# Performance work log

Measured on AMD Instinct MI355X. Metric: run time of the kernel, lower is better.

The kernel has to match this reference:

```python
import jax, jax.numpy as jnp
import numpy as np

ALPHA = 0.2  # LeakyReLU negative slope
NEG_PAD = jnp.float32(-2**31)
N, IN_F, OUT_F = 8192, 512, 64


def setup_inputs() -> dict:
    key = jax.random.key(0)
    k1, k2, k3, k4 = jax.random.split(key, 4)
    h = jax.random.normal(k1, (N, IN_F), dtype=jnp.float32)
    adj = jax.random.randint(k2, (N, N), 0, 2, dtype=jnp.int32)
    # xavier_uniform with gain=1.414
    gain = 1.414
    limW = gain * np.sqrt(6.0 / (IN_F + OUT_F))
    W = jax.random.uniform(k3, (IN_F, OUT_F), dtype=jnp.float32, minval=-limW, maxval=limW)
    lima = gain * np.sqrt(6.0 / (2 * OUT_F + 1))
    a = jax.random.uniform(k4, (2 * OUT_F, 1), dtype=jnp.float32, minval=-lima, maxval=lima)
    return {"h": h, "adj": adj, "W": W, "a": a}


def reference(h, adj, W, a):
    Wh = h @ W                                   # [N, F']
    Wh1 = Wh @ a[:OUT_F, :]                      # [N, 1]
    Wh2 = Wh @ a[OUT_F:, :]                      # [N, 1]
    e = jax.nn.leaky_relu(Wh1 + Wh2.T, negative_slope=ALPHA)  # [N, N]
    attention = jnp.where(adj > 0, e, NEG_PAD)
    attention = jax.nn.softmax(attention, axis=1)
    # dropout in eval mode -> identity
    h_prime = attention @ Wh                     # [N, F']
    return jax.nn.elu(h_prime)                   # concat=True branch
```

## Files before the change

### kernel.cpp

```cpp
#include <hip/hip_runtime.h>
#include <cstdint>
#include <cstddef>

#define LRALPHA 0.2f

typedef _Float16 half8 __attribute__((ext_vector_type(8)));
typedef float f32x4 __attribute__((ext_vector_type(4)));

__global__ __launch_bounds__(256) void k1_wh(
    const float* __restrict__ h, const float* __restrict__ W, const float* __restrict__ a,
    _Float16* __restrict__ whT, float* __restrict__ wh1, float* __restrict__ wh2)
{
  __shared__ __align__(16) float h_lds[32][34];
  __shared__ __align__(16) float w_lds[32][64];
  __shared__ __align__(16) _Float16 whT_l[64][32];

  const int t = threadIdx.x;
  const int tx = t & 15, ty = t >> 4;
  const int i0 = blockIdx.x * 32;

  const int hrow = t >> 3, hk4 = (t & 7) * 4;
  const int wk = t >> 3, wc = (t & 7) * 8;

  float acc00 = 0, acc01 = 0, acc02 = 0, acc03 = 0;
  float acc10 = 0, acc11 = 0, acc12 = 0, acc13 = 0;

  float4 hv  = *reinterpret_cast<const float4*>(&h[(size_t)(i0 + hrow) * 512 + hk4]);
  float4 wv0 = *reinterpret_cast<const float4*>(&W[(size_t)wk * 64 + wc]);
  float4 wv1 = *reinterpret_cast<const float4*>(&W[(size_t)wk * 64 + wc + 4]);

  for (int k0 = 0; k0 < 512; k0 += 32) {
    h_lds[hk4 + 0][hrow] = hv.x;
    h_lds[hk4 + 1][hrow] = hv.y;
    h_lds[hk4 + 2][hrow] = hv.z;
    h_lds[hk4 + 3][hrow] = hv.w;
    *reinterpret_cast<float4*>(&w_lds[wk][wc])     = wv0;
    *reinterpret_cast<float4*>(&w_lds[wk][wc + 4]) = wv1;
    __syncthreads();
    if (k0 + 32 < 512) {
      hv  = *reinterpret_cast<const float4*>(&h[(size_t)(i0 + hrow) * 512 + k0 + 32 + hk4]);
      wv0 = *reinterpret_cast<const float4*>(&W[(size_t)(k0 + 32 + wk) * 64 + wc]);
      wv1 = *reinterpret_cast<const float4*>(&W[(size_t)(k0 + 32 + wk) * 64 + wc + 4]);
    }
#pragma unroll
    for (int kk = 0; kk < 32; ++kk) {
      float2 av = *reinterpret_cast<const float2*>(&h_lds[kk][ty * 2]);
      float4 bv = *reinterpret_cast<const float4*>(&w_lds[kk][tx * 4]);
      acc00 += av.x * bv.x; acc01 += av.x * bv.y; acc02 += av.x * bv.z; acc03 += av.x * bv.w;
      acc10 += av.y * bv.x; acc11 += av.y * bv.y; acc12 += av.y * bv.z; acc13 += av.y * bv.w;
    }
    __syncthreads();
  }

  const float a10 = a[tx * 4 + 0], a11 = a[tx * 4 + 1], a12 = a[tx * 4 + 2], a13 = a[tx * 4 + 3];
  const float a20 = a[64 + tx * 4 + 0], a21 = a[64 + tx * 4 + 1], a22 = a[64 + tx * 4 + 2], a23 = a[64 + tx * 4 + 3];
  float s1_0 = acc00 * a10 + acc01 * a11 + acc02 * a12 + acc03 * a13;
  float s1_1 = acc10 * a10 + acc11 * a11 + acc12 * a12 + acc13 * a13;
  float s2_0 = acc00 * a20 + acc01 * a21 + acc02 * a22 + acc03 * a23;
  float s2_1 = acc10 * a20 + acc11 * a21 + acc12 * a22 + acc13 * a23;
#pragma unroll
  for (int m = 1; m < 16; m <<= 1) {
    s1_0 += __shfl_xor(s1_0, m); s1_1 += __shfl_xor(s1_1, m);
    s2_0 += __shfl_xor(s2_0, m); s2_1 += __shfl_xor(s2_1, m);
  }
  if (tx == 0) {
    wh1[i0 + ty * 2 + 0] = s1_0; wh1[i0 + ty * 2 + 1] = s1_1;
    wh2[i0 + ty * 2 + 0] = s2_0; wh2[i0 + ty * 2 + 1] = s2_1;
  }

  whT_l[tx * 4 + 0][ty * 2 + 0] = (_Float16)acc00;
  whT_l[tx * 4 + 1][ty * 2 + 0] = (_Float16)acc01;
  whT_l[tx * 4 + 2][ty * 2 + 0] = (_Float16)acc02;
  whT_l[tx * 4 + 3][ty * 2 + 0] = (_Float16)acc03;
  whT_l[tx * 4 + 0][ty * 2 + 1] = (_Float16)acc10;
  whT_l[tx * 4 + 1][ty * 2 + 1] = (_Float16)acc11;
  whT_l[tx * 4 + 2][ty * 2 + 1] = (_Float16)acc12;
  whT_l[tx * 4 + 3][ty * 2 + 1] = (_Float16)acc13;
  __syncthreads();
  {
    const int c = t >> 2, r8 = (t & 3) * 8;
    half8 v = *reinterpret_cast<const half8*>(&whT_l[c][r8]);
    *reinterpret_cast<half8*>(&whT[(size_t)c * 8192 + i0 + r8]) = v;
  }
}

__global__ __launch_bounds__(256) void k1b_max(const float* __restrict__ wh2,
                                               float* __restrict__ G)
{
  const int t = threadIdx.x;
  float m = -1e30f;
  for (int i = t; i < 8192; i += 256) m = fmaxf(m, wh2[i]);
#pragma unroll
  for (int mask = 32; mask >= 1; mask >>= 1) m = fmaxf(m, __shfl_xor(m, mask));
  __shared__ float wm[4];
  if ((t & 63) == 0) wm[t >> 6] = m;
  __syncthreads();
  if (t == 0) G[0] = fmaxf(fmaxf(wm[0], wm[1]), fmaxf(wm[2], wm[3]));
}

__global__ __launch_bounds__(256) void k2_attn(
    const int* __restrict__ adj, const _Float16* __restrict__ whT,
    const float* __restrict__ wh1, const float* __restrict__ wh2,
    const float* __restrict__ Gp, float* __restrict__ out)
{
  __shared__ __align__(16) float Osm[4][16][64];
  __shared__ float Dsm[4][16];

  const int t = threadIdx.x;
  const int lane = t & 63;
  const int w = t >> 6;
  const int c = lane & 15;
  const int ks = lane >> 4;
  const int i0 = blockIdx.x * 16;

  const float Gv = Gp[0];
  const float w1r = wh1[i0 + c];
  const float mx = w1r + Gv;
  const float mh = fmaxf(mx, LRALPHA * mx);

  const int*      adjp = adj + (size_t)(i0 + c) * 8192 + w * 2048 + ks * 8;
  const float*    wh2p = wh2 + w * 2048 + ks * 8;
  const _Float16* bp0  = whT + (size_t)c * 8192 + w * 2048 + ks * 8;
  const _Float16* bp1  = bp0 + (size_t)16 * 8192;
  const _Float16* bp2  = bp0 + (size_t)32 * 8192;
  const _Float16* bp3  = bp0 + (size_t)48 * 8192;

  f32x4 acc0 = {0.f,0.f,0.f,0.f}, acc1 = {0.f,0.f,0.f,0.f};
  f32x4 acc2 = {0.f,0.f,0.f,0.f}, acc3 = {0.f,0.f,0.f,0.f};
  float ps = 0.f;

  int4 Aa0, Aa1, Ba0, Ba1;
  float4 Aw0, Aw1, Bw0, Bw1;
  half8 Ab0, Ab1, Ab2, Ab3, Bb0, Bb1, Bb2, Bb3;

#define LOADSET(P, CI) do { const int jj_ = (CI) * 32;                          \
    P##a0 = *reinterpret_cast<const int4*>(adjp + jj_);                         \
    P##a1 = *reinterpret_cast<const int4*>(adjp + jj_ + 4);                     \
    P##w0 = *reinterpret_cast<const float4*>(wh2p + jj_);                       \
    P##w1 = *reinterpret_cast<const float4*>(wh2p + jj_ + 4);                   \
    P##b0 = *reinterpret_cast<const half8*>(bp0 + jj_);                         \
    P##b1 = *reinterpret_cast<const half8*>(bp1 + jj_);                         \
    P##b2 = *reinterpret_cast<const half8*>(bp2 + jj_);                         \
    P##b3 = *reinterpret_cast<const half8*>(bp3 + jj_); } while (0)

#define BODY(P, NEXTCI) do {                                                    \
    const int4 ca0 = P##a0, ca1 = P##a1;                                        \
    const float4 cw0 = P##w0, cw1 = P##w1;                                      \
    const half8 cb0 = P##b0, cb1 = P##b1, cb2 = P##b2, cb3 = P##b3;             \
    if ((NEXTCI) < 64) LOADSET(P, NEXTCI);                                      \
    half8 af;                                                                   \
    { float s_ = w1r + cw0.x; s_ = fmaxf(s_, LRALPHA*s_);                       \
      float p_ = (ca0.x > 0) ? __expf(s_ - mh) : 0.f; ps += p_; af[0] = (_Float16)p_; } \
    { float s_ = w1r + cw0.y; s_ = fmaxf(s_, LRALPHA*s_);                       \
      float p_ = (ca0.y > 0) ? __expf(s_ - mh) : 0.f; ps += p_; af[1] = (_Float16)p_; } \
    { float s_ = w1r + cw0.z; s_ = fmaxf(s_, LRALPHA*s_);                       \
      float p_ = (ca0.z > 0) ? __expf(s_ - mh) : 0.f; ps += p_; af[2] = (_Float16)p_; } \
    { float s_ = w1r + cw0.w; s_ = fmaxf(s_, LRALPHA*s_);                       \
      float p_ = (ca0.w > 0) ? __expf(s_ - mh) : 0.f; ps += p_; af[3] = (_Float16)p_; } \
    { float s_ = w1r + cw1.x; s_ = fmaxf(s_, LRALPHA*s_);                       \
      float p_ = (ca1.x > 0) ? __expf(s_ - mh) : 0.f; ps += p_; af[4] = (_Float16)p_; } \
    { float s_ = w1r + cw1.y; s_ = fmaxf(s_, LRALPHA*s_);                       \
      float p_ = (ca1.y > 0) ? __expf(s_ - mh) : 0.f; ps += p_; af[5] = (_Float16)p_; } \
    { float s_ = w1r + cw1.z; s_ = fmaxf(s_, LRALPHA*s_);                       \
      float p_ = (ca1.z > 0) ? __expf(s_ - mh) : 0.f; ps += p_; af[6] = (_Float16)p_; } \
    { float s_ = w1r + cw1.w; s_ = fmaxf(s_, LRALPHA*s_);                       \
      float p_ = (ca1.w > 0) ? __expf(s_ - mh) : 0.f; ps += p_; af[7] = (_Float16)p_; } \
    acc0 = __builtin_amdgcn_mfma_f32_16x16x32_f16(af, cb0, acc0, 0, 0, 0);      \
    acc1 = __builtin_amdgcn_mfma_f32_16x16x32_f16(af, cb1, acc1, 0, 0, 0);      \
    acc2 = __builtin_amdgcn_mfma_f32_16x16x32_f16(af, cb2, acc2, 0, 0, 0);      \
    acc3 = __builtin_amdgcn_mfma_f32_16x16x32_f16(af, cb3, acc3, 0, 0, 0);      \
  } while (0)

  LOADSET(A, 0);
  LOADSET(B, 1);

  for (int ci = 0; ci < 64; ci += 2) {
    BODY(A, ci + 2);
    BODY(B, ci + 3);
  }
#undef BODY
#undef LOADSET

  float r = ps;
  r += __shfl_xor(r, 16);
  r += __shfl_xor(r, 32);
  if (ks == 0) Dsm[w][c] = r;

#pragma unroll
  for (int q = 0; q < 4; ++q) {
    Osm[w][ks * 4 + q][ 0 + c] = acc0[q];
    Osm[w][ks * 4 + q][16 + c] = acc1[q];
    Osm[w][ks * 4 + q][32 + c] = acc2[q];
    Osm[w][ks * 4 + q][48 + c] = acc3[q];
  }
  __syncthreads();

  {
    const int row = t >> 4, c4 = (t & 15) * 4;
    float4 v0 = *reinterpret_cast<const float4*>(&Osm[0][row][c4]);
    float4 v1 = *reinterpret_cast<const float4*>(&Osm[1][row][c4]);
    float4 v2 = *reinterpret_cast<const float4*>(&Osm[2][row][c4]);
    float4 v3 = *reinterpret_cast<const float4*>(&Osm[3][row][c4]);
    const float d = Dsm[0][row] + Dsm[1][row] + Dsm[2][row] + Dsm[3][row];
    const float inv = 1.0f / d;
    float4 o;
    o.x = (v0.x + v1.x + v2.x + v3.x) * inv;
    o.y = (v0.y + v1.y + v2.y + v3.y) * inv;
    o.z = (v0.z + v1.z + v2.z + v3.z) * inv;
    o.w = (v0.w + v1.w + v2.w + v3.w) * inv;
    o.x = o.x > 0.f ? o.x : __expf(o.x) - 1.f;
    o.y = o.y > 0.f ? o.y : __expf(o.y) - 1.f;
    o.z = o.z > 0.f ? o.z : __expf(o.z) - 1.f;
    o.w = o.w > 0.f ? o.w : __expf(o.w) - 1.f;
    *reinterpret_cast<float4*>(&out[(size_t)(i0 + row) * 64 + c4]) = o;
  }
}

extern "C" void kernel_launch(void* const* d_in, const int* in_sizes, int n_in,
                              void* d_out, int out_size, void* d_ws, size_t ws_size,
                              hipStream_t stream) {
  const float* h   = (const float*)d_in[0];
  const int*   adj = (const int*)d_in[1];
  const float* W   = (const float*)d_in[2];
  const float* a   = (const float*)d_in[3];
  float* out = (float*)d_out;

  char* ws = (char*)d_ws;
  _Float16* whT = (_Float16*)ws;
  float* wh1 = (float*)(ws + (1 << 20));
  float* wh2 = (float*)(ws + (1 << 20) + 32768);
  float* G   = (float*)(ws + (1 << 20) + 65536);

  k1_wh<<<dim3(256), dim3(256), 0, stream>>>(h, W, a, whT, wh1, wh2);
  k1b_max<<<dim3(1), dim3(256), 0, stream>>>(wh2, G);
  k2_attn<<<dim3(512), dim3(256), 0, stream>>>(adj, whT, wh1, wh2, G, out);
}
```

Before: 133.5 us.

## Split attention neighbour range across blocks and combine partials in separate kernel

Each k2_attn block now runs 8 waves over 128 rows and a single quarter of the neighbour (j) range, so all waves in a block share the same whT and wh2 slice. Previously each block's 4 waves covered 16 rows across all four j quarters. Unnormalized output and denominator partials go to global workspace, and a new k3_combine kernel sums the four partials and applies the normalization and ELU. The aim is better cache reuse of the B operand and wh2. The cost is an extra kernel launch and roughly 8 MB of partial writes plus reads.

```diff
diff --git a/kernel.cpp b/kernel.cpp
--- a/kernel.cpp
+++ b/kernel.cpp
@@ -98,29 +98,28 @@
   if (t == 0) G[0] = fmaxf(fmaxf(wm[0], wm[1]), fmaxf(wm[2], wm[3]));
 }
 
-__global__ __launch_bounds__(256) void k2_attn(
+__global__ __launch_bounds__(512) void k2_attn(
     const int* __restrict__ adj, const _Float16* __restrict__ whT,
     const float* __restrict__ wh1, const float* __restrict__ wh2,
-    const float* __restrict__ Gp, float* __restrict__ out)
-{
-  __shared__ __align__(16) float Osm[4][16][64];
-  __shared__ float Dsm[4][16];
-
+    const float* __restrict__ Gp, float* __restrict__ Opart, float* __restrict__ Dpart)
+{
   const int t = threadIdx.x;
   const int lane = t & 63;
   const int w = t >> 6;
   const int c = lane & 15;
   const int ks = lane >> 4;
-  const int i0 = blockIdx.x * 16;
+  const int bj = blockIdx.x & 3;
+  const int bi = blockIdx.x >> 2;
+  const int row0 = bi * 128 + w * 16;
 
   const float Gv = Gp[0];
-  const float w1r = wh1[i0 + c];
+  const float w1r = wh1[row0 + c];
   const float mx = w1r + Gv;
   const float mh = fmaxf(mx, LRALPHA * mx);
 
-  const int*      adjp = adj + (size_t)(i0 + c) * 8192 + w * 2048 + ks * 8;
-  const float*    wh2p = wh2 + w * 2048 + ks * 8;
-  const _Float16* bp0  = whT + (size_t)c * 8192 + w * 2048 + ks * 8;
+  const int*      adjp = adj + (size_t)(row0 + c) * 8192 + bj * 2048 + ks * 8;
+  const float*    wh2p = wh2 + bj * 2048 + ks * 8;
+  const _Float16* bp0  = whT + (size_t)c * 8192 + bj * 2048 + ks * 8;
   const _Float16* bp1  = bp0 + (size_t)16 * 8192;
   const _Float16* bp2  = bp0 + (size_t)32 * 8192;
   const _Float16* bp3  = bp0 + (size_t)48 * 8192;
@@ -184,36 +183,44 @@
   float r = ps;
   r += __shfl_xor(r, 16);
   r += __shfl_xor(r, 32);
-  if (ks == 0) Dsm[w][c] = r;
-
+  if (ks == 0) Dpart[(size_t)bj * 8192 + row0 + c] = r;
+
+  float* ob = Opart + ((size_t)bj * 8192 + row0 + ks * 4) * 64;
 #pragma unroll
   for (int q = 0; q < 4; ++q) {
-    Osm[w][ks * 4 + q][ 0 + c] = acc0[q];
-    Osm[w][ks * 4 + q][16 + c] = acc1[q];
-    Osm[w][ks * 4 + q][32 + c] = acc2[q];
-    Osm[w][ks * 4 + q][48 + c] = acc3[q];
-  }
-  __syncthreads();
-
-  {
-    const int row = t >> 4, c4 = (t & 15) * 4;
-    float4 v0 = *reinterpret_cast<const float4*>(&Osm[0][row][c4]);
-    float4 v1 = *reinterpret_cast<const float4*>(&Osm[1][row][c4]);
-    float4 v2 = *reinterpret_cast<const float4*>(&Osm[2][row][c4]);
-    float4 v3 = *reinterpret_cast<const float4*>(&Osm[3][row][c4]);
-    const float d = Dsm[0][row] + Dsm[1][row] + Dsm[2][row] + Dsm[3][row];
-    const float inv = 1.0f / d;
-    float4 o;
-    o.x = (v0.x + v1.x + v2.x + v3.x) * inv;
-    o.y = (v0.y + v1.y + v2.y + v3.y) * inv;
-    o.z = (v0.z + v1.z + v2.z + v3.z) * inv;
-    o.w = (v0.w + v1.w + v2.w + v3.w) * inv;
-    o.x = o.x > 0.f ? o.x : __expf(o.x) - 1.f;
-    o.y = o.y > 0.f ? o.y : __expf(o.y) - 1.f;
-    o.z = o.z > 0.f ? o.z : __expf(o.z) - 1.f;
-    o.w = o.w > 0.f ? o.w : __expf(o.w) - 1.f;
-    *reinterpret_cast<float4*>(&out[(size_t)(i0 + row) * 64 + c4]) = o;
-  }
+    ob[(size_t)q * 64 +  0 + c] = acc0[q];
+    ob[(size_t)q * 64 + 16 + c] = acc1[q];
+    ob[(size_t)q * 64 + 32 + c] = acc2[q];
+    ob[(size_t)q * 64 + 48 + c] = acc3[q];
+  }
+}
+
+__global__ __launch_bounds__(256) void k3_combine(
+    const float* __restrict__ Opart, const float* __restrict__ Dpart,
+    float* __restrict__ out)
+{
+  const int idx = blockIdx.x * 256 + threadIdx.x;
+  const int row = idx >> 4, c4 = (idx & 15) * 4;
+
+  const float d = Dpart[row] + Dpart[8192 + row] + Dpart[2 * 8192 + row] + Dpart[3 * 8192 + row];
+  const float inv = 1.0f / d;
+
+  const size_t o = (size_t)row * 64 + c4;
+  float4 v0 = *reinterpret_cast<const float4*>(&Opart[o]);
+  float4 v1 = *reinterpret_cast<const float4*>(&Opart[(size_t)8192 * 64 + o]);
+  float4 v2 = *reinterpret_cast<const float4*>(&Opart[(size_t)2 * 8192 * 64 + o]);
+  float4 v3 = *reinterpret_cast<const float4*>(&Opart[(size_t)3 * 8192 * 64 + o]);
+
+  float4 r;
+  r.x = (v0.x + v1.x + v2.x + v3.x) * inv;
+  r.y = (v0.y + v1.y + v2.y + v3.y) * inv;
+  r.z = (v0.z + v1.z + v2.z + v3.z) * inv;
+  r.w = (v0.w + v1.w + v2.w + v3.w) * inv;
+  r.x = r.x > 0.f ? r.x : __expf(r.x) - 1.f;
+  r.y = r.y > 0.f ? r.y : __expf(r.y) - 1.f;
+  r.z = r.z > 0.f ? r.z : __expf(r.z) - 1.f;
+  r.w = r.w > 0.f ? r.w : __expf(r.w) - 1.f;
+  *reinterpret_cast<float4*>(&out[o]) = r;
 }
 
 extern "C" void kernel_launch(void* const* d_in, const int* in_sizes, int n_in,
@@ -227,11 +234,14 @@
 
   char* ws = (char*)d_ws;
   _Float16* whT = (_Float16*)ws;
-  float* wh1 = (float*)(ws + (1 << 20));
-  float* wh2 = (float*)(ws + (1 << 20) + 32768);
-  float* G   = (float*)(ws + (1 << 20) + 65536);
+  float* wh1  = (float*)(ws + 0x100000);
+  float* wh2  = (float*)(ws + 0x108000);
+  float* G    = (float*)(ws + 0x110000);
+  float* Dpart = (float*)(ws + 0x110100);
+  float* Opart = (float*)(ws + 0x140000);
 
   k1_wh<<<dim3(256), dim3(256), 0, stream>>>(h, W, a, whT, wh1, wh2);
   k1b_max<<<dim3(1), dim3(256), 0, stream>>>(wh2, G);
-  k2_attn<<<dim3(512), dim3(256), 0, stream>>>(adj, whT, wh1, wh2, G, out);
-}
+  k2_attn<<<dim3(256), dim3(512), 0, stream>>>(adj, whT, wh1, wh2, G, Opart, Dpart);
+  k3_combine<<<dim3(512), dim3(256), 0, stream>>>(Opart, Dpart, out);
+}
```

Result: no change. 132.8 us (-0.5%).

## Bit-pack adjacency in a pre-pass and read compact mask in attention kernel

Applied to the files above, without the earlier changes.

Adds a pre-pass that compresses the int32 adjacency matrix into one bit per entry, so the attention kernel reads an 8 MB mask instead of the full int matrix. The fp16 Wh transpose is stored in a swizzled chunk layout so each wave's B-operand loads are contiguous. The attention kernel moves to 512 threads with 8 waves splitting the key dimension. The full adjacency is still read once by the pack kernel, and an extra launch plus mask write is added.

```diff
diff --git a/kernel.cpp b/kernel.cpp
--- a/kernel.cpp
+++ b/kernel.cpp
@@ -7,9 +7,25 @@
 typedef _Float16 half8 __attribute__((ext_vector_type(8)));
 typedef float f32x4 __attribute__((ext_vector_type(4)));
 
+__global__ __launch_bounds__(256) void k0_bitpack(const int* __restrict__ adj,
+                                                  unsigned char* __restrict__ bits8)
+{
+  const int nb = 8192 * 1024;
+  const int stride = gridDim.x * 256;
+  for (int b = blockIdx.x * 256 + threadIdx.x; b < nb; b += stride) {
+    const int4* p = reinterpret_cast<const int4*>(adj + (size_t)b * 8);
+    const int4 x = p[0], y = p[1];
+    unsigned m = (x.x > 0 ? 1u : 0u) | (x.y > 0 ? 2u : 0u)
+               | (x.z > 0 ? 4u : 0u) | (x.w > 0 ? 8u : 0u)
+               | (y.x > 0 ? 16u : 0u) | (y.y > 0 ? 32u : 0u)
+               | (y.z > 0 ? 64u : 0u) | (y.w > 0 ? 128u : 0u);
+    bits8[b] = (unsigned char)m;
+  }
+}
+
 __global__ __launch_bounds__(256) void k1_wh(
     const float* __restrict__ h, const float* __restrict__ W, const float* __restrict__ a,
-    _Float16* __restrict__ whT, float* __restrict__ wh1, float* __restrict__ wh2)
+    _Float16* __restrict__ whTsw, float* __restrict__ wh1, float* __restrict__ wh2)
 {
   __shared__ __align__(16) float h_lds[32][34];
   __shared__ __align__(16) float w_lds[32][64];
@@ -78,9 +94,9 @@
   whT_l[tx * 4 + 3][ty * 2 + 1] = (_Float16)acc13;
   __syncthreads();
   {
-    const int c = t >> 2, r8 = (t & 3) * 8;
-    half8 v = *reinterpret_cast<const half8*>(&whT_l[c][r8]);
-    *reinterpret_cast<half8*>(&whT[(size_t)c * 8192 + i0 + r8]) = v;
+    const int cp = t >> 6, cc = (t >> 2) & 15, ks = t & 3;
+    half8 v = *reinterpret_cast<const half8*>(&whT_l[cp * 16 + cc][ks * 8]);
+    *reinterpret_cast<half8*>(&whTsw[(size_t)(i0 >> 5) * 2048 + cp * 512 + (cc * 4 + ks) * 8]) = v;
   }
 }
 
@@ -98,13 +114,13 @@
   if (t == 0) G[0] = fmaxf(fmaxf(wm[0], wm[1]), fmaxf(wm[2], wm[3]));
 }
 
-__global__ __launch_bounds__(256) void k2_attn(
-    const int* __restrict__ adj, const _Float16* __restrict__ whT,
+__global__ __launch_bounds__(512) void k2_attn(
+    const unsigned char* __restrict__ bits8, const _Float16* __restrict__ whTsw,
     const float* __restrict__ wh1, const float* __restrict__ wh2,
     const float* __restrict__ Gp, float* __restrict__ out)
 {
-  __shared__ __align__(16) float Osm[4][16][64];
-  __shared__ float Dsm[4][16];
+  __shared__ __align__(16) float Osm[8][16][64];
+  __shared__ float Dsm[8][16];
 
   const int t = threadIdx.x;
   const int lane = t & 63;
@@ -118,53 +134,49 @@
   const float mx = w1r + Gv;
   const float mh = fmaxf(mx, LRALPHA * mx);
 
-  const int*      adjp = adj + (size_t)(i0 + c) * 8192 + w * 2048 + ks * 8;
-  const float*    wh2p = wh2 + w * 2048 + ks * 8;
-  const _Float16* bp0  = whT + (size_t)c * 8192 + w * 2048 + ks * 8;
-  const _Float16* bp1  = bp0 + (size_t)16 * 8192;
-  const _Float16* bp2  = bp0 + (size_t)32 * 8192;
-  const _Float16* bp3  = bp0 + (size_t)48 * 8192;
+  const unsigned char* mp = bits8 + (size_t)(i0 + c) * 1024 + w * 128 + ks;
+  const float* wh2p = wh2 + w * 1024 + ks * 8;
+  const _Float16* bp = whTsw + (size_t)(w * 32) * 2048 + (c * 4 + ks) * 8;
 
   f32x4 acc0 = {0.f,0.f,0.f,0.f}, acc1 = {0.f,0.f,0.f,0.f};
   f32x4 acc2 = {0.f,0.f,0.f,0.f}, acc3 = {0.f,0.f,0.f,0.f};
   float ps = 0.f;
 
-  int4 Aa0, Aa1, Ba0, Ba1;
+  unsigned Am, Bm;
   float4 Aw0, Aw1, Bw0, Bw1;
   half8 Ab0, Ab1, Ab2, Ab3, Bb0, Bb1, Bb2, Bb3;
 
-#define LOADSET(P, CI) do { const int jj_ = (CI) * 32;                          \
-    P##a0 = *reinterpret_cast<const int4*>(adjp + jj_);                         \
-    P##a1 = *reinterpret_cast<const int4*>(adjp + jj_ + 4);                     \
-    P##w0 = *reinterpret_cast<const float4*>(wh2p + jj_);                       \
-    P##w1 = *reinterpret_cast<const float4*>(wh2p + jj_ + 4);                   \
-    P##b0 = *reinterpret_cast<const half8*>(bp0 + jj_);                         \
-    P##b1 = *reinterpret_cast<const half8*>(bp1 + jj_);                         \
-    P##b2 = *reinterpret_cast<const half8*>(bp2 + jj_);                         \
-    P##b3 = *reinterpret_cast<const half8*>(bp3 + jj_); } while (0)
+#define LOADSET(P, CI) do {                                                     \
+    P##m  = mp[(CI) * 4];                                                       \
+    P##w0 = *reinterpret_cast<const float4*>(wh2p + (CI) * 32);                 \
+    P##w1 = *reinterpret_cast<const float4*>(wh2p + (CI) * 32 + 4);             \
+    P##b0 = *reinterpret_cast<const half8*>(bp + (size_t)(CI) * 2048);          \
+    P##b1 = *reinterpret_cast<const half8*>(bp + (size_t)(CI) * 2048 + 512);    \
+    P##b2 = *reinterpret_cast<const half8*>(bp + (size_t)(CI) * 2048 + 1024);   \
+    P##b3 = *reinterpret_cast<const half8*>(bp + (size_t)(CI) * 2048 + 1536); } while (0)
 
 #define BODY(P, NEXTCI) do {                                                    \
-    const int4 ca0 = P##a0, ca1 = P##a1;                                        \
+    const unsigned cm = P##m;                                                   \
     const float4 cw0 = P##w0, cw1 = P##w1;                                      \
     const half8 cb0 = P##b0, cb1 = P##b1, cb2 = P##b2, cb3 = P##b3;             \
-    if ((NEXTCI) < 64) LOADSET(P, NEXTCI);                                      \
+    if ((NEXTCI) < 32) LOADSET(P, NEXTCI);                                      \
     half8 af;                                                                   \
     { float s_ = w1r + cw0.x; s_ = fmaxf(s_, LRALPHA*s_);                       \
-      float p_ = (ca0.x > 0) ? __expf(s_ - mh) : 0.f; ps += p_; af[0] = (_Float16)p_; } \
+      float p_ = (cm & 1u)   ? __expf(s_ - mh) : 0.f; ps += p_; af[0] = (_Float16)p_; } \
     { float s_ = w1r + cw0.y; s_ = fmaxf(s_, LRALPHA*s_);                       \
-      float p_ = (ca0.y > 0) ? __expf(s_ - mh) : 0.f; ps += p_; af[1] = (_Float16)p_; } \
+      float p_ = (cm & 2u)   ? __expf(s_ - mh) : 0.f; ps += p_; af[1] = (_Float16)p_; } \
     { float s_ = w1r + cw0.z; s_ = fmaxf(s_, LRALPHA*s_);                       \
-      float p_ = (ca0.z > 0) ? __expf(s_ - mh) : 0.f; ps += p_; af[2] = (_Float16)p_; } \
+      float p_ = (cm & 4u)   ? __expf(s_ - mh) : 0.f; ps += p_; af[2] = (_Float16)p_; } \
     { float s_ = w1r + cw0.w; s_ = fmaxf(s_, LRALPHA*s_);                       \
-      float p_ = (ca0.w > 0) ? __expf(s_ - mh) : 0.f; ps += p_; af[3] = (_Float16)p_; } \
+      float p_ = (cm & 8u)   ? __expf(s_ - mh) : 0.f; ps += p_; af[3] = (_Float16)p_; } \
     { float s_ = w1r + cw1.x; s_ = fmaxf(s_, LRALPHA*s_);                       \
-      float p_ = (ca1.x > 0) ? __expf(s_ - mh) : 0.f; ps += p_; af[4] = (_Float16)p_; } \
+      float p_ = (cm & 16u)  ? __expf(s_ - mh) : 0.f; ps += p_; af[4] = (_Float16)p_; } \
     { float s_ = w1r + cw1.y; s_ = fmaxf(s_, LRALPHA*s_);                       \
-      float p_ = (ca1.y > 0) ? __expf(s_ - mh) : 0.f; ps += p_; af[5] = (_Float16)p_; } \
+      float p_ = (cm & 32u)  ? __expf(s_ - mh) : 0.f; ps += p_; af[5] = (_Float16)p_; } \
     { float s_ = w1r + cw1.z; s_ = fmaxf(s_, LRALPHA*s_);                       \
-      float p_ = (ca1.z > 0) ? __expf(s_ - mh) : 0.f; ps += p_; af[6] = (_Float16)p_; } \
+      float p_ = (cm & 64u)  ? __expf(s_ - mh) : 0.f; ps += p_; af[6] = (_Float16)p_; } \
     { float s_ = w1r + cw1.w; s_ = fmaxf(s_, LRALPHA*s_);                       \
-      float p_ = (ca1.w > 0) ? __expf(s_ - mh) : 0.f; ps += p_; af[7] = (_Float16)p_; } \
+      float p_ = (cm & 128u) ? __expf(s_ - mh) : 0.f; ps += p_; af[7] = (_Float16)p_; } \
     acc0 = __builtin_amdgcn_mfma_f32_16x16x32_f16(af, cb0, acc0, 0, 0, 0);      \
     acc1 = __builtin_amdgcn_mfma_f32_16x16x32_f16(af, cb1, acc1, 0, 0, 0);      \
     acc2 = __builtin_amdgcn_mfma_f32_16x16x32_f16(af, cb2, acc2, 0, 0, 0);      \
@@ -174,7 +186,7 @@
   LOADSET(A, 0);
   LOADSET(B, 1);
 
-  for (int ci = 0; ci < 64; ci += 2) {
+  for (int ci = 0; ci < 32; ci += 2) {
     BODY(A, ci + 2);
     BODY(B, ci + 3);
   }
@@ -196,23 +208,20 @@
   __syncthreads();
 
   {
-    const int row = t >> 4, c4 = (t & 15) * 4;
-    float4 v0 = *reinterpret_cast<const float4*>(&Osm[0][row][c4]);
-    float4 v1 = *reinterpret_cast<const float4*>(&Osm[1][row][c4]);
-    float4 v2 = *reinterpret_cast<const float4*>(&Osm[2][row][c4]);
-    float4 v3 = *reinterpret_cast<const float4*>(&Osm[3][row][c4]);
-    const float d = Dsm[0][row] + Dsm[1][row] + Dsm[2][row] + Dsm[3][row];
+    const int row = t >> 5, c2 = (t & 31) * 2;
+    float d = 0.f, sx = 0.f, sy = 0.f;
+#pragma unroll
+    for (int ww = 0; ww < 8; ++ww) {
+      d  += Dsm[ww][row];
+      float2 v = *reinterpret_cast<const float2*>(&Osm[ww][row][c2]);
+      sx += v.x; sy += v.y;
+    }
     const float inv = 1.0f / d;
-    float4 o;
-    o.x = (v0.x + v1.x + v2.x + v3.x) * inv;
-    o.y = (v0.y + v1.y + v2.y + v3.y) * inv;
-    o.z = (v0.z + v1.z + v2.z + v3.z) * inv;
-    o.w = (v0.w + v1.w + v2.w + v3.w) * inv;
-    o.x = o.x > 0.f ? o.x : __expf(o.x) - 1.f;
-    o.y = o.y > 0.f ? o.y : __expf(o.y) - 1.f;
-    o.z = o.z > 0.f ? o.z : __expf(o.z) - 1.f;
-    o.w = o.w > 0.f ? o.w : __expf(o.w) - 1.f;
-    *reinterpret_cast<float4*>(&out[(size_t)(i0 + row) * 64 + c4]) = o;
+    float ox = sx * inv, oy = sy * inv;
+    ox = ox > 0.f ? ox : __expf(ox) - 1.f;
+    oy = oy > 0.f ? oy : __expf(oy) - 1.f;
+    float2 o = {ox, oy};
+    *reinterpret_cast<float2*>(&out[(size_t)(i0 + row) * 64 + c2]) = o;
   }
 }
 
@@ -226,12 +235,14 @@
   float* out = (float*)d_out;
 
   char* ws = (char*)d_ws;
-  _Float16* whT = (_Float16*)ws;
-  float* wh1 = (float*)(ws + (1 << 20));
-  float* wh2 = (float*)(ws + (1 << 20) + 32768);
-  float* G   = (float*)(ws + (1 << 20) + 65536);
-
-  k1_wh<<<dim3(256), dim3(256), 0, stream>>>(h, W, a, whT, wh1, wh2);
+  _Float16* whTsw = (_Float16*)ws;
+  float* wh1 = (float*)(ws + 0x100000);
+  float* wh2 = (float*)(ws + 0x108000);
+  float* G   = (float*)(ws + 0x110000);
+  unsigned char* bits8 = (unsigned char*)(ws + 0x120000);
+
+  k0_bitpack<<<dim3(2048), dim3(256), 0, stream>>>(adj, bits8);
+  k1_wh<<<dim3(256), dim3(256), 0, stream>>>(h, W, a, whTsw, wh1, wh2);
   k1b_max<<<dim3(1), dim3(256), 0, stream>>>(wh2, G);
-  k2_attn<<<dim3(512), dim3(256), 0, stream>>>(adj, whT, wh1, wh2, G, out);
-}
+  k2_attn<<<dim3(512), dim3(512), 0, stream>>>(bits8, whTsw, wh1, wh2, G, out);
+}
```

New measurement: 123.3 us. -7.7%, faster.
